# Kernel tuning notes

Hardware: AMD Instinct MI355X
Metric: run time of the kernel (lower is better)

The kernel has to match this reference:

```python
import jax, jax.numpy as jnp
import numpy as np


def setup_inputs() -> dict:
    key = jax.random.key(0)
    k1, k2, k3, k4 = jax.random.split(key, 4)
    b, c_in, t, h, w = 8, 64, 16, 64, 64
    c_out, kh, kw = 64, 3, 3
    x = jax.random.normal(k1, (b, c_in, t, h, w), dtype=jnp.float32)
    alpha = jax.random.uniform(k2, (b, c_in, t, 1, 1), dtype=jnp.float32)
    fan_in = c_in * kh * kw
    weight = jax.random.normal(k3, (c_out, c_in, kh, kw), dtype=jnp.float32) / np.sqrt(fan_in)
    bias = jax.random.normal(k4, (c_out,), dtype=jnp.float32) * 0.05
    return {"x": x, "alpha": alpha, "weight": weight, "bias": bias}


def reference(x, alpha, weight, bias):
    # x: (b, c_in, t, h, w); alpha: (b, c_in, t, 1, 1)
    # weight: (c_out, c_in, kh, kw); bias: (c_out,)
    b, c_in, t, h, w = x.shape
    c_out, _, kh, kw = weight.shape
    pad = ((kh // 2, kh // 2), (kw // 2, kw // 2))  # padding=1 for 3x3
    # per-(b,t) calibrated weights: alpha scales the c_in dim (cal_dim='cin')
    a = jnp.transpose(alpha[..., 0, 0], (0, 2, 1))          # (b, t, c_in)
    w_bt = a[:, :, None, :, None, None] * weight[None, None]  # (b, t, c_out, c_in, kh, kw)
    xs = jnp.transpose(x, (0, 2, 1, 3, 4)).reshape(b * t, 1, c_in, h, w)
    ws = w_bt.reshape(b * t, c_out, c_in, kh, kw)

    def conv_one(xi, wi):
        return jax.lax.conv_general_dilated(
            xi, wi, window_strides=(1, 1), padding=pad,
            dimension_numbers=("NCHW", "OIHW", "NCHW"))[0]

    out = jax.vmap(conv_one)(xs, ws)                          # (b*t, c_out, h, w)
    out = out + bias[None, :, None, None]
    out = out.reshape(b, t, c_out, h, w).transpose(0, 2, 1, 3, 4)
    return out  # (b, c_out, t, h, w)
```

## Files before the change

kernel.cpp:

```cpp
#include <hip/hip_runtime.h>


#define CIN  64
#define COUT 64
#define TT   16
#define BB   8
#define HH   64
#define WW   64

typedef __attribute__((ext_vector_type(8))) short bf16x8;
typedef __attribute__((ext_vector_type(4))) float f32x4;

__device__ __forceinline__ unsigned short f2bf(float f) {
    union { float f; unsigned u; } v; v.f = f;
    unsigned r = (v.u + 0x7FFF + ((v.u >> 16) & 1)) >> 16;
    return (unsigned short)r;
}

__global__ __launch_bounds__(256) void prep_w(const float* __restrict__ wgt,
                                              unsigned short* __restrict__ wb) {
    int idx = blockIdx.x * 256 + threadIdx.x;
    if (idx < COUT * CIN * 9) {
        int co  = idx / (CIN * 9);
        int r   = idx - co * (CIN * 9);
        int ci  = r / 9;
        int tap = r - ci * 9;
        int q    = co >> 4;
        int co_l = co & 15;
        int kc   = ci >> 5;
        int kg   = (ci >> 3) & 3;
        int e    = ci & 7;
        wb[(((((q * 9 + tap) * 2 + kc) * 4 + kg) * 16) + co_l) * 8 + e] = f2bf(wgt[idx]);
    }
}

__global__ __launch_bounds__(256, 2) void conv5(const float* __restrict__ x,
                                                const float* __restrict__ alpha,
                                                const short* __restrict__ wb,
                                                const float* __restrict__ bias,
                                                float* __restrict__ out) {
    __shared__ __align__(16) short xs[4 * 4224];

    const int orig  = blockIdx.x;
    const int blk   = (orig & 7) * 512 + (orig >> 3);
    const int ytile = blk & 31;
    const int bt    = blk >> 5;
    const int t     = bt & 15;
    const int b     = bt >> 4;
    const int y0    = ytile * 2;
    const int tid   = threadIdx.x;
    const int wv    = tid >> 6;
    const int lane  = tid & 63;
    const int co_l  = lane & 15;
    const int kg    = lane >> 4;
    const int mg    = wv >> 1;
    const int rw    = wv & 1;

    bf16x8 wreg[2][9][2];
#pragma unroll
    for (int m = 0; m < 2; ++m)
#pragma unroll
        for (int tap = 0; tap < 9; ++tap)
#pragma unroll
            for (int kc = 0; kc < 2; ++kc)
                wreg[m][tap][kc] = *(const bf16x8*)(
                    wb + ((((mg * 2 + m) * 9 + tap) * 2 + kc) * 64 + lane) * 8);

    {
        const int ci0 = wv * 16;
        if (lane < 16) {
            int4 z = {0, 0, 0, 0};
            *(int4*)(xs + wv * 4224 + (lane >> 3) * 4160 + (lane & 7) * 8) = z;
        }
#pragma unroll
        for (int r = 0; r < 4; ++r) {
            const int gy = y0 - 1 + r;
            short* rowb = xs + r * 4224;
#pragma unroll
            for (int gi = 0; gi < 2; ++gi) {
                const int g  = wv * 2 + gi;
                const int cg = ci0 + gi * 8;
                int4 o = {0, 0, 0, 0};
                if ((unsigned)gy < HH) {
                    const float* p = x + ((size_t)((b * CIN + cg) * TT + t) * HH + gy) * WW + lane;
                    float v0 = p[0 * 65536] * alpha[(b * CIN + cg + 0) * TT + t];
                    float v1 = p[1 * 65536] * alpha[(b * CIN + cg + 1) * TT + t];
                    float v2 = p[2 * 65536] * alpha[(b * CIN + cg + 2) * TT + t];
                    float v3 = p[3 * 65536] * alpha[(b * CIN + cg + 3) * TT + t];
                    float v4 = p[4 * 65536] * alpha[(b * CIN + cg + 4) * TT + t];
                    float v5 = p[5 * 65536] * alpha[(b * CIN + cg + 5) * TT + t];
                    float v6 = p[6 * 65536] * alpha[(b * CIN + cg + 6) * TT + t];
                    float v7 = p[7 * 65536] * alpha[(b * CIN + cg + 7) * TT + t];
                    o.x = (int)f2bf(v0) | ((int)f2bf(v1) << 16);
                    o.y = (int)f2bf(v2) | ((int)f2bf(v3) << 16);
                    o.z = (int)f2bf(v4) | ((int)f2bf(v5) << 16);
                    o.w = (int)f2bf(v6) | ((int)f2bf(v7) << 16);
                }
                *(int4*)(rowb + (lane + 1) * 64 + ((g ^ (lane & 7)) * 8)) = o;
            }
        }
    }
    __syncthreads();

    f32x4 acc[2][4] = {};
    int si[3][2];
#pragma unroll
    for (int dxi = 0; dxi < 3; ++dxi)
#pragma unroll
        for (int kc = 0; kc < 2; ++kc) {
            int wx = co_l + dxi - 1;
            si[dxi][kc] = (wx + 1) * 64 + (((kc * 4 + kg) ^ (wx & 7)) * 8);
        }

#pragma unroll
    for (int tap = 0; tap < 9; ++tap) {
        const int ky  = tap / 3;
        const int dxi = tap - 3 * ky;
        const short* rowp = xs + (rw + ky) * 4224;
#pragma unroll
        for (int kc = 0; kc < 2; ++kc) {
            const short* bp = rowp + si[dxi][kc];
#pragma unroll
            for (int n = 0; n < 4; ++n) {
                bf16x8 bfr = *(const bf16x8*)(bp + n * 1024);
                acc[0][n] = __builtin_amdgcn_mfma_f32_16x16x32_bf16(
                    wreg[0][tap][kc], bfr, acc[0][n], 0, 0, 0);
                acc[1][n] = __builtin_amdgcn_mfma_f32_16x16x32_bf16(
                    wreg[1][tap][kc], bfr, acc[1][n], 0, 0, 0);
            }
        }
    }

    const int y = y0 + rw;
#pragma unroll
    for (int m = 0; m < 2; ++m) {
#pragma unroll
        for (int rr = 0; rr < 4; ++rr) {
            const int co = (mg * 2 + m) * 16 + kg * 4 + rr;
            const float bv = bias[co];
            float* op = out + (size_t)(((b * COUT + co) * TT + t) * HH + y) * WW;
#pragma unroll
            for (int n = 0; n < 4; ++n)
                op[n * 16 + co_l] = acc[m][n][rr] + bv;
        }
    }
}

extern "C" void kernel_launch(void* const* d_in, const int* in_sizes, int n_in,
                              void* d_out, int out_size, void* d_ws, size_t ws_size,
                              hipStream_t stream) {
    const float* x      = (const float*)d_in[0];
    const float* alpha  = (const float*)d_in[1];
    const float* weight = (const float*)d_in[2];
    const float* bias   = (const float*)d_in[3];
    float* out          = (float*)d_out;

    unsigned short* wb = (unsigned short*)d_ws;

    hipLaunchKernelGGL(prep_w, dim3(144), dim3(256), 0, stream, weight, wb);
    hipLaunchKernelGGL(conv5, dim3(BB * TT * (HH / 2)), dim3(256), 0, stream,
                       x, alpha, (const short*)wb, bias, out);
}
```

Measured before the change: 278.0 us.

## Persist blocks over 16-row strips with a ring-buffered, prefetched input pipeline

Each block now handles 16 output rows of one (b,t) slice instead of 2, keeping weights in registers across 8 iterations. An 8-slot LDS ring buffer reuses halo rows across iterations, and global loads for the next two rows are issued before the MFMA loop so they overlap compute. Alpha is hoisted into scalar registers and s_setprio is raised during the MFMA section. The grid shrinks to 512 blocks, which reduces weight reloads and redundant halo loads but lowers parallelism and adds register pressure from the prefetch buffers.

Result: faster. 269.1 us (-3.2%).

```diff
diff --git a/kernel.cpp b/kernel.cpp
--- a/kernel.cpp
+++ b/kernel.cpp
@@ -7,6 +7,7 @@
 #define BB   8
 #define HH   64
 #define WW   64
+#define NSTEP 8
 
 typedef __attribute__((ext_vector_type(8))) short bf16x8;
 typedef __attribute__((ext_vector_type(4))) float f32x4;
@@ -34,27 +35,27 @@
     }
 }
 
-__global__ __launch_bounds__(256, 2) void conv5(const float* __restrict__ x,
+__global__ __launch_bounds__(256, 2) void conv6(const float* __restrict__ x,
                                                 const float* __restrict__ alpha,
                                                 const short* __restrict__ wb,
                                                 const float* __restrict__ bias,
                                                 float* __restrict__ out) {
-    __shared__ __align__(16) short xs[4 * 4224];
+    __shared__ __align__(16) short xs[8 * 4224];
 
-    const int orig  = blockIdx.x;
-    const int blk   = (orig & 7) * 512 + (orig >> 3);
-    const int ytile = blk & 31;
-    const int bt    = blk >> 5;
-    const int t     = bt & 15;
-    const int b     = bt >> 4;
-    const int y0    = ytile * 2;
-    const int tid   = threadIdx.x;
-    const int wv    = tid >> 6;
-    const int lane  = tid & 63;
-    const int co_l  = lane & 15;
-    const int kg    = lane >> 4;
-    const int mg    = wv >> 1;
-    const int rw    = wv & 1;
+    const int orig = blockIdx.x;
+    const int blk  = (orig & 7) * 64 + (orig >> 3);
+    const int qy   = blk & 3;
+    const int bt   = blk >> 2;
+    const int t    = bt & 15;
+    const int b    = bt >> 4;
+    const int yb   = qy * 16;
+    const int tid  = threadIdx.x;
+    const int wv   = tid >> 6;
+    const int lane = tid & 63;
+    const int co_l = lane & 15;
+    const int kg   = lane >> 4;
+    const int mg   = wv >> 1;
+    const int rw   = wv & 1;
 
     bf16x8 wreg[2][9][2];
 #pragma unroll
@@ -66,43 +67,58 @@
                 wreg[m][tap][kc] = *(const bf16x8*)(
                     wb + ((((mg * 2 + m) * 9 + tap) * 2 + kc) * 64 + lane) * 8);
 
-    {
-        const int ci0 = wv * 16;
-        if (lane < 16) {
-            int4 z = {0, 0, 0, 0};
-            *(int4*)(xs + wv * 4224 + (lane >> 3) * 4160 + (lane & 7) * 8) = z;
+    float av[2][8];
+#pragma unroll
+    for (int gi = 0; gi < 2; ++gi)
+#pragma unroll
+        for (int j = 0; j < 8; ++j) {
+            float a = alpha[(b * CIN + (wv + gi * 4) * 8 + j) * TT + t];
+            av[gi][j] = __builtin_bit_cast(
+                float, __builtin_amdgcn_readfirstlane(__builtin_bit_cast(int, a)));
         }
+
+    const float* xbase0 = x + (size_t)((b * CIN + wv * 8) * TT + t) * (HH * WW);
+    const float* xbase1 = x + (size_t)((b * CIN + (wv + 4) * 8) * TT + t) * (HH * WW);
+
+    if (tid < 128) {
+        int slot = tid >> 4, col = (tid >> 3) & 1, sg = tid & 7;
+        int4 z = {0, 0, 0, 0};
+        *(int4*)(xs + slot * 4224 + col * 4160 + sg * 8) = z;
+    }
+
+    float fb[2][2][8];
+    auto stage_load = [&](int gy0) {
 #pragma unroll
-        for (int r = 0; r < 4; ++r) {
-            const int gy = y0 - 1 + r;
-            short* rowb = xs + r * 4224;
+        for (int r = 0; r < 2; ++r) {
+            const int gy = gy0 + r;
+            const bool ok = (unsigned)gy < HH;
+            const float* p0 = xbase0 + gy * WW + lane;
+            const float* p1 = xbase1 + gy * WW + lane;
+#pragma unroll
+            for (int j = 0; j < 8; ++j) {
+                fb[r][0][j] = ok ? p0[j * 65536] : 0.0f;
+                fb[r][1][j] = ok ? p1[j * 65536] : 0.0f;
+            }
+        }
+    };
+    auto stage_store = [&](int s0) {
+#pragma unroll
+        for (int r = 0; r < 2; ++r)
 #pragma unroll
             for (int gi = 0; gi < 2; ++gi) {
-                const int g  = wv * 2 + gi;
-                const int cg = ci0 + gi * 8;
-                int4 o = {0, 0, 0, 0};
-                if ((unsigned)gy < HH) {
-                    const float* p = x + ((size_t)((b * CIN + cg) * TT + t) * HH + gy) * WW + lane;
-                    float v0 = p[0 * 65536] * alpha[(b * CIN + cg + 0) * TT + t];
-                    float v1 = p[1 * 65536] * alpha[(b * CIN + cg + 1) * TT + t];
-                    float v2 = p[2 * 65536] * alpha[(b * CIN + cg + 2) * TT + t];
-                    float v3 = p[3 * 65536] * alpha[(b * CIN + cg + 3) * TT + t];
-                    float v4 = p[4 * 65536] * alpha[(b * CIN + cg + 4) * TT + t];
-                    float v5 = p[5 * 65536] * alpha[(b * CIN + cg + 5) * TT + t];
-                    float v6 = p[6 * 65536] * alpha[(b * CIN + cg + 6) * TT + t];
-                    float v7 = p[7 * 65536] * alpha[(b * CIN + cg + 7) * TT + t];
-                    o.x = (int)f2bf(v0) | ((int)f2bf(v1) << 16);
-                    o.y = (int)f2bf(v2) | ((int)f2bf(v3) << 16);
-                    o.z = (int)f2bf(v4) | ((int)f2bf(v5) << 16);
-                    o.w = (int)f2bf(v6) | ((int)f2bf(v7) << 16);
-                }
-                *(int4*)(rowb + (lane + 1) * 64 + ((g ^ (lane & 7)) * 8)) = o;
+                const int g = wv + gi * 4;
+                int4 o;
+                o.x = (int)f2bf(fb[r][gi][0] * av[gi][0]) | ((int)f2bf(fb[r][gi][1] * av[gi][1]) << 16);
+                o.y = (int)f2bf(fb[r][gi][2] * av[gi][2]) | ((int)f2bf(fb[r][gi][3] * av[gi][3]) << 16);
+                o.z = (int)f2bf(fb[r][gi][4] * av[gi][4]) | ((int)f2bf(fb[r][gi][5] * av[gi][5]) << 16);
+                o.w = (int)f2bf(fb[r][gi][6] * av[gi][6]) | ((int)f2bf(fb[r][gi][7] * av[gi][7]) << 16);
+                *(int4*)(xs + ((s0 + r) & 7) * 4224 + (lane + 1) * 64 + ((g ^ (lane & 7)) * 8)) = o;
             }
-        }
-    }
-    __syncthreads();
+    };
 
-    f32x4 acc[2][4] = {};
+    stage_load(yb - 1); stage_store(0);
+    stage_load(yb + 1); stage_store(2);
+
     int si[3][2];
 #pragma unroll
     for (int dxi = 0; dxi < 3; ++dxi)
@@ -112,37 +128,48 @@
             si[dxi][kc] = (wx + 1) * 64 + (((kc * 4 + kg) ^ (wx & 7)) * 8);
         }
 
+    __syncthreads();
+
+    for (int it = 0; it < NSTEP; ++it) {
+        if (it < NSTEP - 1) stage_load(yb + 2 * it + 3);
+
+        f32x4 acc[2][4] = {};
+        __builtin_amdgcn_s_setprio(1);
 #pragma unroll
-    for (int tap = 0; tap < 9; ++tap) {
-        const int ky  = tap / 3;
-        const int dxi = tap - 3 * ky;
-        const short* rowp = xs + (rw + ky) * 4224;
+        for (int tap = 0; tap < 9; ++tap) {
+            const int ky  = tap / 3;
+            const int dxi = tap - 3 * ky;
+            const short* rowp = xs + ((2 * it + rw + ky) & 7) * 4224;
 #pragma unroll
-        for (int kc = 0; kc < 2; ++kc) {
-            const short* bp = rowp + si[dxi][kc];
+            for (int kc = 0; kc < 2; ++kc) {
+                const short* bp = rowp + si[dxi][kc];
 #pragma unroll
-            for (int n = 0; n < 4; ++n) {
-                bf16x8 bfr = *(const bf16x8*)(bp + n * 1024);
-                acc[0][n] = __builtin_amdgcn_mfma_f32_16x16x32_bf16(
-                    wreg[0][tap][kc], bfr, acc[0][n], 0, 0, 0);
-                acc[1][n] = __builtin_amdgcn_mfma_f32_16x16x32_bf16(
-                    wreg[1][tap][kc], bfr, acc[1][n], 0, 0, 0);
+                for (int n = 0; n < 4; ++n) {
+                    bf16x8 bfr = *(const bf16x8*)(bp + n * 1024);
+                    acc[0][n] = __builtin_amdgcn_mfma_f32_16x16x32_bf16(
+                        wreg[0][tap][kc], bfr, acc[0][n], 0, 0, 0);
+                    acc[1][n] = __builtin_amdgcn_mfma_f32_16x16x32_bf16(
+                        wreg[1][tap][kc], bfr, acc[1][n], 0, 0, 0);
+                }
             }
         }
-    }
+        __builtin_amdgcn_s_setprio(0);
 
-    const int y = y0 + rw;
+        const int y = yb + 2 * it + rw;
 #pragma unroll
-    for (int m = 0; m < 2; ++m) {
+        for (int m = 0; m < 2; ++m)
 #pragma unroll
-        for (int rr = 0; rr < 4; ++rr) {
-            const int co = (mg * 2 + m) * 16 + kg * 4 + rr;
-            const float bv = bias[co];
-            float* op = out + (size_t)(((b * COUT + co) * TT + t) * HH + y) * WW;
+            for (int rr = 0; rr < 4; ++rr) {
+                const int co = (mg * 2 + m) * 16 + kg * 4 + rr;
+                const float bv = bias[co];
+                float* op = out + (size_t)(((b * COUT + co) * TT + t) * HH + y) * WW;
 #pragma unroll
-            for (int n = 0; n < 4; ++n)
-                op[n * 16 + co_l] = acc[m][n][rr] + bv;
-        }
+                for (int n = 0; n < 4; ++n)
+                    op[n * 16 + co_l] = acc[m][n][rr] + bv;
+            }
+
+        if (it < NSTEP - 1) stage_store(2 * it + 4);
+        __syncthreads();
     }
 }
 
@@ -158,6 +185,6 @@
     unsigned short* wb = (unsigned short*)d_ws;
 
     hipLaunchKernelGGL(prep_w, dim3(144), dim3(256), 0, stream, weight, wb);
-    hipLaunchKernelGGL(conv5, dim3(BB * TT * (HH / 2)), dim3(256), 0, stream,
+    hipLaunchKernelGGL(conv6, dim3(8 * 64), dim3(256), 0, stream,
                        x, alpha, (const short*)wb, bias, out);
 }
```
